# Kernel optimization log

Hardware: AMD Instinct MI355X
Metric: run time of the kernel (lower is better)

Reference implementation:

```python
import jax, jax.numpy as jnp
import numpy as np

EPS = 1e-5

def _conv(x, w, pad):
    # x: [B,C,H,W] NCHW, w: [O,I,kh,kw] OIHW
    return jax.lax.conv_general_dilated(
        x, w, (1, 1), [(pad, pad), (pad, pad)],
        dimension_numbers=('NCHW', 'OIHW', 'NCHW'))

def _bn(x, g, b, m, v):
    # eval-mode batchnorm folded into scale/shift
    s = g * jax.lax.rsqrt(v + EPS)
    return x * s[None, :, None, None] + (b - m * s)[None, :, None, None]

def _cbr(x, w, g, b, m, v):
    # Convolution block from CornerNet: conv3x3(pad=1, no bias) + BN + ReLU
    return jax.nn.relu(_bn(_conv(x, w, 1), g, b, m, v))


def setup_inputs() -> dict:
    key = jax.random.key(0)
    B, Cin, C, H, W = 4, 256, 256, 128, 128
    kdims = {'up': (C, Cin, 3, 3), 'down': (C, Cin, 3, 3),
             'p': (C, C, 3, 3), 'c1': (C, Cin, 1, 1), 'c2': (C, C, 3, 3)}
    inp = {'x': jax.random.normal(key, (B, Cin, H, W), dtype=jnp.float32)}
    for i, n in enumerate(['up', 'down', 'p', 'c1', 'c2']):
        ks = jax.random.split(jax.random.fold_in(key, i + 1), 5)
        inp['w_' + n] = jax.random.normal(ks[0], kdims[n], dtype=jnp.float32) * 0.02
        inp['g_' + n] = 1.0 + 0.1 * jax.random.normal(ks[1], (C,), dtype=jnp.float32)
        inp['b_' + n] = 0.1 * jax.random.normal(ks[2], (C,), dtype=jnp.float32)
        inp['m_' + n] = 0.1 * jax.random.normal(ks[3], (C,), dtype=jnp.float32)
        inp['v_' + n] = 0.5 + jax.random.uniform(ks[4], (C,), dtype=jnp.float32)
    return inp


def reference(x,
              w_up, g_up, b_up, m_up, v_up,
              w_down, g_down, b_down, m_down, v_down,
              w_p, g_p, b_p, m_p, v_p,
              w_c1, g_c1, b_c1, m_c1, v_c1,
              w_c2, g_c2, b_c2, m_c2, v_c2):
    # up branch: conv-bn-relu then LeftPool (reverse cummax over W) then RightPool (cummax over W)
    up = _cbr(x, w_up, g_up, b_up, m_up, v_up)
    up = jax.lax.cummax(up, axis=3, reverse=True)   # LeftPool
    up = jax.lax.cummax(up, axis=3)                 # RightPool
    # down branch: conv-bn-relu then TopPool (reverse cummax over H) then BottomPool (cummax over H)
    down = _cbr(x, w_down, g_down, b_down, m_down, v_down)
    down = jax.lax.cummax(down, axis=2, reverse=True)  # TopPool
    down = jax.lax.cummax(down, axis=2)                # BottomPool
    # merge path: 3x3 conv + BN on pooled sum
    merge = _bn(_conv(up + down, w_p, 1), g_p, b_p, m_p, v_p)
    # shortcut path: 1x1 conv + BN on input
    bn1 = _bn(_conv(x, w_c1, 0), g_c1, b_c1, m_c1, v_c1)
    relu1 = jax.nn.relu(merge + bn1)
    # output Convolution block
    return _cbr(relu1, w_c2, g_c2, b_c2, m_c2, v_c2)
```

## Files before the change

### kernel.cpp

```cpp
#include <hip/hip_runtime.h>

typedef unsigned short u16;
typedef __attribute__((ext_vector_type(8))) short bf16x8;
typedef __attribute__((ext_vector_type(4))) float f32x4;


__device__ __forceinline__ u16 f2bf(float f) {
  unsigned u = __float_as_uint(f);
  unsigned r = u + 0x7fffu + ((u >> 16) & 1u);
  return (u16)(r >> 16);
}

__device__ __forceinline__ void gll16(const char* g, char* l) {
  __builtin_amdgcn_global_load_lds((const __attribute__((address_space(1))) void*)g,
                                   (__attribute__((address_space(3))) void*)l, 16, 0, 0);
}

__global__ void bn_prep_kernel(const float* __restrict__ g, const float* __restrict__ b,
                               const float* __restrict__ m, const float* __restrict__ v,
                               float* __restrict__ st) {
  int c = threadIdx.x;
  float s = g[c] * rsqrtf(v[c] + 1e-5f);
  st[c] = s;
  st[256 + c] = b[c] - m[c] * s;
}

__global__ void bn_fix_kernel(float* __restrict__ st) {
  int c = threadIdx.x;
  st[2 * 512 + 256 + c] += st[3 * 512 + 256 + c];
  st[3 * 512 + c] = st[3 * 512 + c] / st[2 * 512 + c];
}

__global__ void wprep3_kernel(const float* __restrict__ w, u16* __restrict__ dst) {
  int idx = blockIdx.x * 256 + threadIdx.x;
  int e = idx & 7, lane = (idx >> 3) & 63, f = (idx >> 9) & 3, coq = (idx >> 11) & 1;
  int blk = idx >> 12;
  int cohalf = blk / 72, step = blk % 72;
  int outer = step / 12, rr = step % 12, dwi = rr >> 2, kc = rr & 3;
  int half = outer / 3, d = outer % 3;
  int s = d * 3 + dwi;
  int co = cohalf * 128 + coq * 64 + f * 16 + (lane & 15);
  int ci = half * 128 + kc * 32 + (lane >> 4) * 8 + e;
  dst[idx] = f2bf(w[(co * 256 + ci) * 9 + s]);
}

__global__ void wprep1_kernel(const float* __restrict__ w, u16* __restrict__ dst,
                              const float* __restrict__ ratio) {
  int idx = blockIdx.x * 256 + threadIdx.x;
  int e = idx & 7, lane = (idx >> 3) & 63, f = (idx >> 9) & 3, coq = (idx >> 11) & 1;
  int blk = idx >> 12;
  int cohalf = blk >> 3, step = blk & 7;
  int half2 = step >> 2, kc = step & 3;
  int co = cohalf * 128 + coq * 64 + f * 16 + (lane & 15);
  int ci = half2 * 128 + kc * 32 + (lane >> 4) * 8 + e;
  dst[idx] = f2bf(w[co * 256 + ci] * ratio[co]);
}

__global__ __launch_bounds__(256) void nchw_to_nhwc_kernel(const float* __restrict__ x,
                                                           char* __restrict__ xb) {
  __shared__ __align__(16) u16 tl[128 * 130];
  int bh = blockIdx.x; int b = bh >> 7, h = bh & 127;
  int t = threadIdx.x;
  for (int half = 0; half < 2; ++half) {
    __syncthreads();
    for (int i = 0; i < 64; ++i) {
      int cil = i * 2 + (t >> 7);
      int ci = half * 128 + cil;
      int w = t & 127;
      tl[w * 130 + cil] = f2bf(x[(size_t)((b * 256 + ci) * 128 + h) * 128 + w]);
    }
    __syncthreads();
    char* plane = xb + (size_t)(b * 128 + h) * 65536 + half * 32768;
    for (int i = 0; i < 32; ++i) {
      int w = i * 4 + (t >> 6);
      int c2 = (t & 63) * 2;
      unsigned v = *(const unsigned*)&tl[w * 130 + c2];
      *(unsigned*)(plane + w * 256 + ((c2 * 2) ^ (((w + 1) & 7) << 4))) = v;
    }
  }
}

__device__ __forceinline__ void stage_b(const char* plane, char* ldsB, int t) {
  if (plane) {
    char* dst = ldsB + 256 + t * 16;
    const char* g = plane + t * 16;
#pragma unroll
    for (int r = 0; r < 8; ++r) gll16(g + r * 4096, dst + r * 4096);
  } else {
    int4 z = {0, 0, 0, 0};
#pragma unroll
    for (int r = 0; r < 8; ++r) *(int4*)(ldsB + 256 + r * 4096 + t * 16) = z;
  }
}

__device__ __forceinline__ const char* a_src(const char* wA1, const char* wA2, int step,
                                             int coq, int lane) {
  const char* src = (step < 72) ? (wA1 + (size_t)step * 8192)
                                : (wA2 + (size_t)(step - 72) * 8192);
  return src + coq * 4096 + lane * 16;
}

__device__ __forceinline__ void conv_pipeline(const char* inB1, const char* inB2,
                                              const char* wA1, const char* wA2,
                                              int h, int nsteps, char* lds,
                                              f32x4 (&acc)[4][4]) {
  const int t = threadIdx.x;
  const int wv = t >> 6, lane = t & 63;
  const int lane15 = lane & 15, q = lane >> 4;
  const int coq = wv >> 1, wh = wv & 1;
  char* ldsB = lds;

  int wpb[4];
#pragma unroll
  for (int f = 0; f < 4; ++f) wpb[f] = wh * 64 + f * 16 + lane15;

  {
    int4 z = {0, 0, 0, 0};
    if (t < 16) *(int4*)(ldsB + t * 16) = z;
    else if (t < 32) *(int4*)(ldsB + 33024 + (t - 16) * 16) = z;
  }

  bf16x8 aCur[4], aNxt[4];
  {
    const char* p = a_src(wA1, wA2, 0, coq, lane);
#pragma unroll
    for (int f = 0; f < 4; ++f) aCur[f] = *(const bf16x8*)(p + f * 1024);
  }

  int i = 0;
  for (int outer = 0; outer < 6; ++outer) {
    const int half = (outer >= 3) ? 1 : 0;
    const int d = outer - half * 3;
    const int hs = h + d - 1;
    const char* plane = (hs >= 0 && hs < 128)
                            ? inB1 + (size_t)hs * 65536 + (size_t)half * 32768
                            : nullptr;
    stage_b(plane, ldsB, t);
    __syncthreads();
#pragma unroll
    for (int dwi = 0; dwi < 3; ++dwi)
#pragma unroll
      for (int kc = 0; kc < 4; ++kc) {
        int ns = (i + 1 < nsteps) ? i + 1 : 0;
        const char* p = a_src(wA1, wA2, ns, coq, lane);
#pragma unroll
        for (int f = 0; f < 4; ++f) aNxt[f] = *(const bf16x8*)(p + f * 1024);
        bf16x8 bf[4];
#pragma unroll
        for (int f = 0; f < 4; ++f) {
          int wp = wpb[f] + dwi;
          bf[f] = *(const bf16x8*)(ldsB + wp * 256 + ((kc * 64 + q * 16) ^ ((wp & 7) << 4)));
        }
#pragma unroll
        for (int fm = 0; fm < 4; ++fm)
#pragma unroll
          for (int fn = 0; fn < 4; ++fn)
            acc[fm][fn] = __builtin_amdgcn_mfma_f32_16x16x32_bf16(aCur[fm], bf[fn], acc[fm][fn], 0, 0, 0);
#pragma unroll
        for (int f = 0; f < 4; ++f) aCur[f] = aNxt[f];
        ++i;
      }
    __syncthreads();
  }
  if (nsteps > 72) {
    for (int half2 = 0; half2 < 2; ++half2) {
      stage_b(inB2 + (size_t)h * 65536 + (size_t)half2 * 32768, ldsB, t);
      __syncthreads();
#pragma unroll
      for (int kc = 0; kc < 4; ++kc) {
        int ns = (i + 1 < nsteps) ? i + 1 : 0;
        const char* p = a_src(wA1, wA2, ns, coq, lane);
#pragma unroll
        for (int f = 0; f < 4; ++f) aNxt[f] = *(const bf16x8*)(p + f * 1024);
        bf16x8 bf[4];
#pragma unroll
        for (int f = 0; f < 4; ++f) {
          int wp = wpb[f] + 1;
          bf[f] = *(const bf16x8*)(ldsB + wp * 256 + ((kc * 64 + q * 16) ^ ((wp & 7) << 4)));
        }
#pragma unroll
        for (int fm = 0; fm < 4; ++fm)
#pragma unroll
          for (int fn = 0; fn < 4; ++fn)
            acc[fm][fn] = __builtin_amdgcn_mfma_f32_16x16x32_bf16(aCur[fm], bf[fn], acc[fm][fn], 0, 0, 0);
#pragma unroll
        for (int f = 0; f < 4; ++f) aCur[f] = aNxt[f];
        ++i;
      }
      __syncthreads();
    }
  }
}

__device__ __forceinline__ void zero_acc(f32x4 (&acc)[4][4]) {
  f32x4 z = {0.f, 0.f, 0.f, 0.f};
#pragma unroll
  for (int i = 0; i < 4; ++i)
#pragma unroll
    for (int j = 0; j < 4; ++j) acc[i][j] = z;
}

__device__ __forceinline__ void store_pad_relu(f32x4 (&acc)[4][4], const float* __restrict__ st,
                                               int cohalf, int b, int h, char* __restrict__ out) {
  const int t = threadIdx.x, lane = t & 63, wv = t >> 6;
  const int lane15 = lane & 15, q = lane >> 4, coq = wv >> 1, wh = wv & 1;
  char* plane = out + (size_t)(b * 128 + h) * 65536 + cohalf * 32768;
#pragma unroll
  for (int fm = 0; fm < 4; ++fm) {
    int co_l = coq * 64 + fm * 16 + q * 4;
    int co = cohalf * 128 + co_l;
    float ss[4], tt[4];
#pragma unroll
    for (int r = 0; r < 4; ++r) { ss[r] = st[co + r]; tt[r] = st[256 + co + r]; }
#pragma unroll
    for (int fn = 0; fn < 4; ++fn) {
      int w = wh * 64 + fn * 16 + lane15;
      short4 o;
      o.x = (short)f2bf(fmaxf(acc[fm][fn][0] * ss[0] + tt[0], 0.f));
      o.y = (short)f2bf(fmaxf(acc[fm][fn][1] * ss[1] + tt[1], 0.f));
      o.z = (short)f2bf(fmaxf(acc[fm][fn][2] * ss[2] + tt[2], 0.f));
      o.w = (short)f2bf(fmaxf(acc[fm][fn][3] * ss[3] + tt[3], 0.f));
      *(short4*)(plane + w * 256 + ((co_l * 2) ^ (((w + 1) & 7) << 4))) = o;
    }
  }
}

__global__ __launch_bounds__(256, 3) void conv_up_kernel(const char* __restrict__ xb,
                                                         const char* __restrict__ wp,
                                                         const float* __restrict__ st,
                                                         float* __restrict__ rmax) {
  __shared__ __align__(16) char lds[33280];
  int swz = (blockIdx.x & 7) * 64 + (blockIdx.x >> 3);
  int b = swz >> 7, h = swz & 127;
  int cohalf = blockIdx.y;
  const char* wA = wp + (size_t)cohalf * 589824;
  f32x4 acc[4][4];
  zero_acc(acc);
  conv_pipeline(xb + (size_t)b * 8388608, nullptr, wA, wA, h, 72, lds, acc);

  const int t = threadIdx.x, lane = t & 63, wv = t >> 6;
  const int lane15 = lane & 15, q = lane >> 4, coq = wv >> 1, wh = wv & 1;
  float* rlds = (float*)lds;
  __syncthreads();
#pragma unroll
  for (int fm = 0; fm < 4; ++fm) {
    int co_l = coq * 64 + fm * 16 + q * 4;
    int co = cohalf * 128 + co_l;
#pragma unroll
    for (int r = 0; r < 4; ++r) {
      float ss = st[co + r], tt = st[256 + co + r];
      float v = 0.f;
#pragma unroll
      for (int fn = 0; fn < 4; ++fn) v = fmaxf(v, acc[fm][fn][r] * ss + tt);
      v = fmaxf(v, __shfl_xor(v, 1));
      v = fmaxf(v, __shfl_xor(v, 2));
      v = fmaxf(v, __shfl_xor(v, 4));
      v = fmaxf(v, __shfl_xor(v, 8));
      if (lane15 == 0) rlds[wh * 128 + co_l + r] = v;
    }
  }
  __syncthreads();
  if (t < 128)
    rmax[(size_t)(b * 128 + h) * 256 + cohalf * 128 + t] = fmaxf(rlds[t], rlds[128 + t]);
}

__global__ __launch_bounds__(256, 3) void conv_down_kernel(const char* __restrict__ xb,
                                                           const char* __restrict__ wp,
                                                           const float* __restrict__ st,
                                                           char* __restrict__ out) {
  __shared__ __align__(16) char lds[33280];
  int swz = (blockIdx.x & 7) * 64 + (blockIdx.x >> 3);
  int b = swz >> 7, h = swz & 127;
  int cohalf = blockIdx.y;
  const char* wA = wp + (size_t)cohalf * 589824;
  f32x4 acc[4][4];
  zero_acc(acc);
  conv_pipeline(xb + (size_t)b * 8388608, nullptr, wA, wA, h, 72, lds, acc);
  store_pad_relu(acc, st, cohalf, b, h, out);
}

__global__ __launch_bounds__(256) void colmax_kernel(const char* __restrict__ dp,
                                                     float* __restrict__ cmax) {
  int bw = blockIdx.x; int b = bw >> 7, w = bw & 127;
  int c = threadIdx.x;
  size_t base = (size_t)b * 8388608 + (size_t)(c >> 7) * 32768 + w * 256 +
                (((c & 127) * 2) ^ (((w + 1) & 7) << 4));
  float m = 0.f;
  for (int h = 0; h < 128; ++h) {
    u16 raw = *(const u16*)(dp + base + (size_t)h * 65536);
    m = fmaxf(m, __uint_as_float(((unsigned)raw) << 16));
  }
  cmax[(size_t)(b * 128 + w) * 256 + c] = m;
}

__global__ __launch_bounds__(256) void pooled_kernel(const float* __restrict__ rmax,
                                                     const float* __restrict__ cmax,
                                                     char* __restrict__ dp) {
  int bh = blockIdx.x; int b = bh >> 7, h = bh & 127;
  int c = threadIdx.x;
  float rm = rmax[(size_t)(b * 128 + h) * 256 + c];
  char* plane = dp + (size_t)(b * 128 + h) * 65536 + (c >> 7) * 32768;
  int cb = (c & 127) * 2;
  for (int w = 0; w < 128; ++w) {
    float v = rm + cmax[(size_t)(b * 128 + w) * 256 + c];
    *(u16*)(plane + w * 256 + (cb ^ (((w + 1) & 7) << 4))) = f2bf(v);
  }
}

__global__ __launch_bounds__(256, 3) void conv_merge_kernel(const char* __restrict__ dp,
                                                            const char* __restrict__ xb,
                                                            const char* __restrict__ wp_p,
                                                            const char* __restrict__ wp_c1,
                                                            const float* __restrict__ st,
                                                            char* __restrict__ out) {
  __shared__ __align__(16) char lds[33280];
  int swz = (blockIdx.x & 7) * 64 + (blockIdx.x >> 3);
  int b = swz >> 7, h = swz & 127;
  int cohalf = blockIdx.y;
  f32x4 acc[4][4];
  zero_acc(acc);
  conv_pipeline(dp + (size_t)b * 8388608, xb + (size_t)b * 8388608,
                wp_p + (size_t)cohalf * 589824, wp_c1 + (size_t)cohalf * 65536,
                h, 80, lds, acc);
  store_pad_relu(acc, st, cohalf, b, h, out);
}

__global__ __launch_bounds__(256, 3) void conv_c2_kernel(const char* __restrict__ relu1,
                                                         const char* __restrict__ wp,
                                                         const float* __restrict__ st,
                                                         float* __restrict__ out) {
  __shared__ __align__(16) char lds[33280];
  int swz = (blockIdx.x & 7) * 64 + (blockIdx.x >> 3);
  int b = swz >> 7, h = swz & 127;
  int cohalf = blockIdx.y;
  const char* wA = wp + (size_t)cohalf * 589824;
  f32x4 acc[4][4];
  zero_acc(acc);
  conv_pipeline(relu1 + (size_t)b * 8388608, nullptr, wA, wA, h, 72, lds, acc);

  const int t = threadIdx.x, lane = t & 63, wv = t >> 6;
  const int lane15 = lane & 15, q = lane >> 4, coq = wv >> 1, wh = wv & 1;
  float* tl = (float*)lds;
  for (int g = 0; g < 8; ++g) {
    __syncthreads();
    if (coq == (g >> 2)) {
      int fm = g & 3;
      int co_l = coq * 64 + fm * 16 + q * 4;
      int co = cohalf * 128 + co_l;
#pragma unroll
      for (int r = 0; r < 4; ++r) {
        float ss = st[co + r], tt = st[256 + co + r];
#pragma unroll
        for (int fn = 0; fn < 4; ++fn) {
          int w = wh * 64 + fn * 16 + lane15;
          tl[(q * 4 + r) * 132 + w] = fmaxf(acc[fm][fn][r] * ss + tt, 0.f);
        }
      }
    }
    __syncthreads();
    int row = t >> 4, ch = t & 15;
    int co = cohalf * 128 + g * 16 + row;
    float* dst = out + (size_t)((b * 256 + co) * 128 + h) * 128 + ch * 8;
    float4 p0 = *(float4*)&tl[row * 132 + ch * 8];
    float4 p1 = *(float4*)&tl[row * 132 + ch * 8 + 4];
    *(float4*)dst = p0;
    *(float4*)(dst + 4) = p1;
  }
}

extern "C" void kernel_launch(void* const* d_in, const int* in_sizes, int n_in,
                              void* d_out, int out_size, void* d_ws, size_t ws_size,
                              hipStream_t stream) {
  (void)in_sizes; (void)n_in; (void)out_size; (void)ws_size;
  const float* x    = (const float*)d_in[0];
  const float* w_up = (const float*)d_in[1];
  const float* w_dn = (const float*)d_in[6];
  const float* w_p  = (const float*)d_in[11];
  const float* w_c1 = (const float*)d_in[16];
  const float* w_c2 = (const float*)d_in[21];

  char* ws = (char*)d_ws;
  char* xb    = ws;
  char* dp    = ws + 33554432ull;
  char* relu1 = ws + 67108864ull;
  char* wp_up = ws + 100663296ull;
  char* wp_dn = ws + 101842944ull;
  char* wp_p  = ws + 103022592ull;
  char* wp_c2 = ws + 104202240ull;
  char* wp_c1 = ws + 105381888ull;
  float* st   = (float*)(ws + 105512960ull);
  float* rmax = (float*)(ws + 105523200ull);
  float* cmax = (float*)(ws + 106047488ull);

  bn_prep_kernel<<<1, 256, 0, stream>>>((const float*)d_in[2], (const float*)d_in[3],
                                        (const float*)d_in[4], (const float*)d_in[5], st);
  bn_prep_kernel<<<1, 256, 0, stream>>>((const float*)d_in[7], (const float*)d_in[8],
                                        (const float*)d_in[9], (const float*)d_in[10], st + 512);
  bn_prep_kernel<<<1, 256, 0, stream>>>((const float*)d_in[12], (const float*)d_in[13],
                                        (const float*)d_in[14], (const float*)d_in[15], st + 1024);
  bn_prep_kernel<<<1, 256, 0, stream>>>((const float*)d_in[17], (const float*)d_in[18],
                                        (const float*)d_in[19], (const float*)d_in[20], st + 1536);
  bn_prep_kernel<<<1, 256, 0, stream>>>((const float*)d_in[22], (const float*)d_in[23],
                                        (const float*)d_in[24], (const float*)d_in[25], st + 2048);
  bn_fix_kernel<<<1, 256, 0, stream>>>(st);

  wprep3_kernel<<<2304, 256, 0, stream>>>(w_up, (u16*)wp_up);
  wprep3_kernel<<<2304, 256, 0, stream>>>(w_dn, (u16*)wp_dn);
  wprep3_kernel<<<2304, 256, 0, stream>>>(w_p, (u16*)wp_p);
  wprep3_kernel<<<2304, 256, 0, stream>>>(w_c2, (u16*)wp_c2);
  wprep1_kernel<<<256, 256, 0, stream>>>(w_c1, (u16*)wp_c1, st + 1536);

  nchw_to_nhwc_kernel<<<512, 256, 0, stream>>>(x, xb);

  conv_up_kernel<<<dim3(512, 2), 256, 0, stream>>>(xb, wp_up, st, rmax);
  conv_down_kernel<<<dim3(512, 2), 256, 0, stream>>>(xb, wp_dn, st + 512, dp);
  colmax_kernel<<<512, 256, 0, stream>>>(dp, cmax);
  pooled_kernel<<<512, 256, 0, stream>>>(rmax, cmax, dp);
  conv_merge_kernel<<<dim3(512, 2), 256, 0, stream>>>(dp, xb, wp_p, wp_c1, st + 1024, relu1);
  conv_c2_kernel<<<dim3(512, 2), 256, 0, stream>>>(relu1, wp_c2, st + 2048, (float*)d_out);
}
```

Before: 460.4 us.

## Deepen weight prefetch to two steps, add MFMA priority, vectorize pooled store

The conv pipeline now prefetches weight fragments two steps ahead with a three-slot register ring instead of one step with a copy, and raises wave priority around the MFMA block. The barrier placement moves from after each compute phase to before each staging phase. Separately, pooled_kernel now writes 16-byte packed bf16 vectors per thread instead of scalar u16 stores. The deeper prefetch adds register pressure under the 3-blocks-per-CU launch bound.

```diff
diff --git a/kernel.cpp b/kernel.cpp
--- a/kernel.cpp
+++ b/kernel.cpp
@@ -93,11 +93,18 @@
   }
 }
 
-__device__ __forceinline__ const char* a_src(const char* wA1, const char* wA2, int step,
-                                             int coq, int lane) {
+__device__ __forceinline__ const char* a_ptr(const char* wA1, const char* wA2, int step, int off) {
   const char* src = (step < 72) ? (wA1 + (size_t)step * 8192)
                                 : (wA2 + (size_t)(step - 72) * 8192);
-  return src + coq * 4096 + lane * 16;
+  return src + off;
+}
+
+__device__ __forceinline__ void zero_acc(f32x4 (&acc)[4][4]) {
+  f32x4 z = {0.f, 0.f, 0.f, 0.f};
+#pragma unroll
+  for (int i = 0; i < 4; ++i)
+#pragma unroll
+    for (int j = 0; j < 4; ++j) acc[i][j] = z;
 }
 
 __device__ __forceinline__ void conv_pipeline(const char* inB1, const char* inB2,
@@ -109,6 +116,7 @@
   const int lane15 = lane & 15, q = lane >> 4;
   const int coq = wv >> 1, wh = wv & 1;
   char* ldsB = lds;
+  const int aoff = coq * 4096 + lane * 16;
 
   int wpb[4];
 #pragma unroll
@@ -120,14 +128,16 @@
     else if (t < 32) *(int4*)(ldsB + 33024 + (t - 16) * 16) = z;
   }
 
-  bf16x8 aCur[4], aNxt[4];
+  bf16x8 aB[3][4];
   {
-    const char* p = a_src(wA1, wA2, 0, coq, lane);
-#pragma unroll
-    for (int f = 0; f < 4; ++f) aCur[f] = *(const bf16x8*)(p + f * 1024);
-  }
-
-  int i = 0;
+    const char* p0 = a_ptr(wA1, wA2, 0, aoff);
+    const char* p1 = a_ptr(wA1, wA2, 1, aoff);
+#pragma unroll
+    for (int f = 0; f < 4; ++f) aB[0][f] = *(const bf16x8*)(p0 + f * 1024);
+#pragma unroll
+    for (int f = 0; f < 4; ++f) aB[1][f] = *(const bf16x8*)(p1 + f * 1024);
+  }
+
   for (int outer = 0; outer < 6; ++outer) {
     const int half = (outer >= 3) ? 1 : 0;
     const int d = outer - half * 3;
@@ -135,69 +145,64 @@
     const char* plane = (hs >= 0 && hs < 128)
                             ? inB1 + (size_t)hs * 65536 + (size_t)half * 32768
                             : nullptr;
+    __syncthreads();
     stage_b(plane, ldsB, t);
     __syncthreads();
 #pragma unroll
-    for (int dwi = 0; dwi < 3; ++dwi)
-#pragma unroll
-      for (int kc = 0; kc < 4; ++kc) {
-        int ns = (i + 1 < nsteps) ? i + 1 : 0;
-        const char* p = a_src(wA1, wA2, ns, coq, lane);
-#pragma unroll
-        for (int f = 0; f < 4; ++f) aNxt[f] = *(const bf16x8*)(p + f * 1024);
-        bf16x8 bf[4];
-#pragma unroll
-        for (int f = 0; f < 4; ++f) {
-          int wp = wpb[f] + dwi;
-          bf[f] = *(const bf16x8*)(ldsB + wp * 256 + ((kc * 64 + q * 16) ^ ((wp & 7) << 4)));
-        }
-#pragma unroll
-        for (int fm = 0; fm < 4; ++fm)
-#pragma unroll
-          for (int fn = 0; fn < 4; ++fn)
-            acc[fm][fn] = __builtin_amdgcn_mfma_f32_16x16x32_bf16(aCur[fm], bf[fn], acc[fm][fn], 0, 0, 0);
-#pragma unroll
-        for (int f = 0; f < 4; ++f) aCur[f] = aNxt[f];
-        ++i;
+    for (int j = 0; j < 12; ++j) {
+      const int dwi = j >> 2, kc = j & 3;
+      const int cb = j % 3, pf = (j + 2) % 3;
+      int sg = outer * 12 + j + 2;
+      if (sg >= nsteps) sg = nsteps - 1;
+      const char* p = a_ptr(wA1, wA2, sg, aoff);
+#pragma unroll
+      for (int f = 0; f < 4; ++f) aB[pf][f] = *(const bf16x8*)(p + f * 1024);
+      bf16x8 bf[4];
+#pragma unroll
+      for (int f = 0; f < 4; ++f) {
+        int wp = wpb[f] + dwi;
+        bf[f] = *(const bf16x8*)(ldsB + wp * 256 + ((kc * 64 + q * 16) ^ ((wp & 7) << 4)));
       }
-    __syncthreads();
+      __builtin_amdgcn_s_setprio(1);
+#pragma unroll
+      for (int fm = 0; fm < 4; ++fm)
+#pragma unroll
+        for (int fn = 0; fn < 4; ++fn)
+          acc[fm][fn] = __builtin_amdgcn_mfma_f32_16x16x32_bf16(aB[cb][fm], bf[fn], acc[fm][fn], 0, 0, 0);
+      __builtin_amdgcn_s_setprio(0);
+    }
   }
   if (nsteps > 72) {
+#pragma unroll
     for (int half2 = 0; half2 < 2; ++half2) {
+      __syncthreads();
       stage_b(inB2 + (size_t)h * 65536 + (size_t)half2 * 32768, ldsB, t);
       __syncthreads();
 #pragma unroll
-      for (int kc = 0; kc < 4; ++kc) {
-        int ns = (i + 1 < nsteps) ? i + 1 : 0;
-        const char* p = a_src(wA1, wA2, ns, coq, lane);
-#pragma unroll
-        for (int f = 0; f < 4; ++f) aNxt[f] = *(const bf16x8*)(p + f * 1024);
+      for (int j2 = 0; j2 < 4; ++j2) {
+        const int jg = half2 * 4 + j2;
+        const int cb = jg % 3, pf = (jg + 2) % 3;
+        int sg = 72 + jg + 2;
+        if (sg >= nsteps) sg = nsteps - 1;
+        const char* p = a_ptr(wA1, wA2, sg, aoff);
+#pragma unroll
+        for (int f = 0; f < 4; ++f) aB[pf][f] = *(const bf16x8*)(p + f * 1024);
         bf16x8 bf[4];
 #pragma unroll
         for (int f = 0; f < 4; ++f) {
           int wp = wpb[f] + 1;
-          bf[f] = *(const bf16x8*)(ldsB + wp * 256 + ((kc * 64 + q * 16) ^ ((wp & 7) << 4)));
+          bf[f] = *(const bf16x8*)(ldsB + wp * 256 + ((j2 * 64 + q * 16) ^ ((wp & 7) << 4)));
         }
+        __builtin_amdgcn_s_setprio(1);
 #pragma unroll
         for (int fm = 0; fm < 4; ++fm)
 #pragma unroll
           for (int fn = 0; fn < 4; ++fn)
-            acc[fm][fn] = __builtin_amdgcn_mfma_f32_16x16x32_bf16(aCur[fm], bf[fn], acc[fm][fn], 0, 0, 0);
-#pragma unroll
-        for (int f = 0; f < 4; ++f) aCur[f] = aNxt[f];
-        ++i;
+            acc[fm][fn] = __builtin_amdgcn_mfma_f32_16x16x32_bf16(aB[cb][fm], bf[fn], acc[fm][fn], 0, 0, 0);
+        __builtin_amdgcn_s_setprio(0);
       }
-      __syncthreads();
-    }
-  }
-}
-
-__device__ __forceinline__ void zero_acc(f32x4 (&acc)[4][4]) {
-  f32x4 z = {0.f, 0.f, 0.f, 0.f};
-#pragma unroll
-  for (int i = 0; i < 4; ++i)
-#pragma unroll
-    for (int j = 0; j < 4; ++j) acc[i][j] = z;
+    }
+  }
 }
 
 __device__ __forceinline__ void store_pad_relu(f32x4 (&acc)[4][4], const float* __restrict__ st,
@@ -297,13 +302,26 @@
                                                      const float* __restrict__ cmax,
                                                      char* __restrict__ dp) {
   int bh = blockIdx.x; int b = bh >> 7, h = bh & 127;
-  int c = threadIdx.x;
-  float rm = rmax[(size_t)(b * 128 + h) * 256 + c];
-  char* plane = dp + (size_t)(b * 128 + h) * 65536 + (c >> 7) * 32768;
-  int cb = (c & 127) * 2;
-  for (int w = 0; w < 128; ++w) {
-    float v = rm + cmax[(size_t)(b * 128 + w) * 256 + c];
-    *(u16*)(plane + w * 256 + (cb ^ (((w + 1) & 7) << 4))) = f2bf(v);
+  int t = threadIdx.x;
+  char* plane = dp + (size_t)(b * 128 + h) * 65536;
+  const float* rm = rmax + (size_t)(b * 128 + h) * 256;
+#pragma unroll
+  for (int it = 0; it < 16; ++it) {
+    int id = it * 256 + t;
+    int half = id >> 11, rem = id & 2047;
+    int w = rem >> 4, slot = rem & 15;
+    int c0 = half * 128 + slot * 8;
+    const float* cm = cmax + (size_t)(b * 128 + w) * 256 + c0;
+    const float* rr = rm + c0;
+    u16 e[8];
+#pragma unroll
+    for (int k = 0; k < 8; ++k) e[k] = f2bf(rr[k] + cm[k]);
+    int4 v;
+    v.x = (int)(e[0] | ((unsigned)e[1] << 16));
+    v.y = (int)(e[2] | ((unsigned)e[3] << 16));
+    v.z = (int)(e[4] | ((unsigned)e[5] << 16));
+    v.w = (int)(e[6] | ((unsigned)e[7] << 16));
+    *(int4*)(plane + half * 32768 + w * 256 + ((slot ^ ((w + 1) & 7)) << 4)) = v;
   }
 }
 
```

Measured after the change: 445.2 us. -3.3%, faster.
